# Optimization experiments

Measured on AMD Instinct MI355X. Metric: run time of the kernel, lower is better.

The kernel has to match this reference:

```python
import jax, jax.numpy as jnp
import numpy as np

N, E, C, A, F = 10000, 128000, 128, 10, 8
LDIMS = (1, 3, 5)  # 0e, 1o, 2e spherical-harmonic block sizes
NPATH = len(LDIMS)


def setup_inputs() -> dict:
    key = jax.random.key(0)
    ks = jax.random.split(key, 16)
    rn = lambda k, s, sc=1.0: jax.random.normal(k, s, dtype=jnp.float32) * sc
    inp = {
        "node_attrs": rn(ks[0], (N, A)),
        "node_feats": rn(ks[1], (N, C)),
        "edge_attrs_real": rn(ks[2], (E, 9)),
        "edge_attrs_imag": rn(ks[3], (E, 9)),
        "edge_feats": jax.random.uniform(ks[4], (E, F), dtype=jnp.float32),
        "edge_index": jax.random.randint(ks[5], (2, E), 0, N, dtype=jnp.int32),
        # learned parameters (e3nn 1/sqrt(fan_in) normalization folded into init)
        "W_up": rn(ks[6], (C, C), 1.0 / np.sqrt(C)),            # o3.Linear on 128x0e
        "W_skip": rn(ks[7], (C, A, C), 1.0 / np.sqrt(C * A)),    # FullyConnectedTensorProduct
        "W_mlp1": rn(ks[8], (F, 64), 1.0 / np.sqrt(F)),
        "W_mlp2": rn(ks[9], (64, 64), 1.0 / 8.0),
        "W_mlp3": rn(ks[10], (64, 64), 1.0 / 8.0),
        "W_mlp4": rn(ks[11], (64, NPATH * C), 1.0 / 8.0),        # -> conv_tp.weight_numel = 384
        "W_lin0": rn(ks[12], (C, C), 1.0 / np.sqrt(C)),          # o3.Linear per-l blocks
        "W_lin1": rn(ks[13], (C, C), 1.0 / np.sqrt(C)),
        "W_lin2": rn(ks[14], (C, C), 1.0 / np.sqrt(C)),
    }
    return inp


def _conv_tp(x, y, w):
    """scalar(128x0e) x sh(0e+1o+2e) uvu tensor product with per-edge weights.
    x: [E,C] sender scalars, y: [E,9] edge sh, w: [E,NPATH,C] -> [E, C*9] irreps_mid layout."""
    outs, off = [], 0
    for l, d in enumerate(LDIMS):
        yl = y[:, off:off + d]                      # [E,d]
        off += d
        xw = x * w[:, l]                            # [E,C]
        outs.append((xw[:, :, None] * yl[:, None, :]).reshape(-1, C * d))
    return jnp.concatenate(outs, axis=-1)           # [E, C*(1+3+5)]


def _linear_irreps(m, Ws):
    """o3.Linear mixing channels within each l block. m: [N, C*9] -> [N, C, 9]."""
    outs, off = [], 0
    for l, d in enumerate(LDIMS):
        blk = m[:, off:off + C * d].reshape(-1, C, d)  # [N,C,d]
        off += C * d
        outs.append(jnp.einsum('num,uk->nkm', blk, Ws[l]))
    return jnp.concatenate(outs, axis=-1)              # [N,C,9] (reshape_irreps layout)


def reference(node_attrs, node_feats, edge_attrs_real, edge_attrs_imag, edge_feats,
              edge_index, W_up, W_skip, W_mlp1, W_mlp2, W_mlp3, W_mlp4,
              W_lin0, W_lin1, W_lin2):
    sender, receiver = edge_index[0], edge_index[1]
    # skip connection: FullyConnectedTensorProduct(node_feats 128x0e, node_attrs 10x0e)
    sc = jnp.einsum('nu,nv,uvk->nk', node_feats, node_attrs, W_skip)
    # linear_up
    h = node_feats @ W_up
    # per-edge tensor-product weights from radial MLP (silu hidden layers, linear out)
    t = jax.nn.silu(edge_feats @ W_mlp1)
    t = jax.nn.silu(t @ W_mlp2)
    t = jax.nn.silu(t @ W_mlp3)
    tpw = (t @ W_mlp4).reshape(-1, NPATH, C)
    # gather senders, tensor product for real and imag edge attrs
    xs = h[sender]
    mji_r = _conv_tp(xs, edge_attrs_real, tpw)
    mji_i = _conv_tp(xs, edge_attrs_imag, tpw)
    # scatter-sum to receivers
    msg_r = jax.ops.segment_sum(mji_r, receiver, num_segments=N)
    msg_i = jax.ops.segment_sum(mji_i, receiver, num_segments=N)
    # output linear + reshape_irreps -> [N, C, 9]
    Ws = (W_lin0, W_lin1, W_lin2)
    out_r = _linear_irreps(msg_r, Ws)
    out_i = _linear_irreps(msg_i, Ws)
    return out_r, out_i, sc
```

## Files before the change

kernel.cpp:

```cpp
#include <hip/hip_runtime.h>
#include <hip/hip_bf16.h>

#define N_NODES 10000
#define N_EDGES 128000
#define C_DIM   128

typedef __attribute__((ext_vector_type(8))) short bf16x8;
typedef __attribute__((ext_vector_type(4))) float f32x4;


__device__ __forceinline__ float silu_f(float x) {
  return x / (1.f + __expf(-x));
}

__device__ __forceinline__ unsigned short f2bf(float x) {
  __hip_bfloat16 b = __float2bfloat16(x);
  return *(unsigned short*)&b;
}

__device__ __forceinline__ float bf2f(unsigned short u) {
  __hip_bfloat16 b = *(__hip_bfloat16*)&u;
  return __bfloat162float(b);
}

__device__ __forceinline__ bf16x8 pack8(float4 lo, float4 hi) {
  bf16x8 r;
  r[0] = (short)f2bf(lo.x); r[1] = (short)f2bf(lo.y);
  r[2] = (short)f2bf(lo.z); r[3] = (short)f2bf(lo.w);
  r[4] = (short)f2bf(hi.x); r[5] = (short)f2bf(hi.y);
  r[6] = (short)f2bf(hi.z); r[7] = (short)f2bf(hi.w);
  return r;
}

#define HB_NODES 40
__global__ __launch_bounds__(256) void k_h(const float* __restrict__ feats,
                                           const float* __restrict__ Wup,
                                           float* __restrict__ h) {
  int tid = threadIdx.x;
  int j = tid & 127;
  int par = tid >> 7;
  int n0 = blockIdx.x * HB_NODES;
  float wreg[128];
  #pragma unroll
  for (int k = 0; k < 128; k++) wreg[k] = Wup[k * 128 + j];
  #pragma unroll 2
  for (int i = par; i < HB_NODES; i += 2) {
    int n = __builtin_amdgcn_readfirstlane(n0 + i);
    const float* fr = &feats[n * 128];
    float acc = 0.f;
    #pragma unroll
    for (int k = 0; k < 128; k++) acc += fr[k] * wreg[k];
    h[n * 128 + j] = acc;
  }
}

__global__ void k_wcvt(const float* __restrict__ Wskip,
                       const float* __restrict__ Wl0,
                       const float* __restrict__ Wl1,
                       const float* __restrict__ Wl2,
                       const float* __restrict__ W1, const float* __restrict__ W2,
                       const float* __restrict__ W3, const float* __restrict__ W4,
                       unsigned short* __restrict__ wbT,
                       unsigned short* __restrict__ wlT,
                       unsigned short* __restrict__ w1f, unsigned short* __restrict__ w2f,
                       unsigned short* __restrict__ w3f, unsigned short* __restrict__ w4f) {
  int idx = blockIdx.x * 256 + threadIdx.x;
  if (idx < 163840) {
    int j = idx >> 7, k = idx & 127;
    int u = j / 10, v = j - u * 10;
    wbT[k * 1280 + v * 128 + u] = f2bf(Wskip[idx]);
  } else if (idx < 212992) {
    int t = idx - 163840;
    int l = t >> 14, r = t & 16383;
    int u = r >> 7, k = r & 127;
    const float* W = (l == 0) ? Wl0 : (l == 1) ? Wl1 : Wl2;
    wlT[(l * 128 + k) * 128 + u] = f2bf(W[r]);
  } else if (idx < 215040) {
    int j = idx - 212992;
    int ct = j >> 9, r = j & 511, n = r >> 5, t = r & 31;
    w1f[j] = (t < 8) ? f2bf(W1[t * 64 + ct * 16 + n]) : (unsigned short)0;
    (void)ct;
    if (t < 8) w1f[j] = f2bf(W1[t * 64 + ct * 16 + n]);
  } else if (idx < 219136) {
    int j = idx - 215040;
    int ctks = j >> 9, r = j & 511, n = r >> 5, t = r & 31;
    int ct = ctks >> 1, ks = ctks & 1;
    w2f[j] = f2bf(W2[(ks * 32 + t) * 64 + ct * 16 + n]);
  } else if (idx < 223232) {
    int j = idx - 219136;
    int ctks = j >> 9, r = j & 511, n = r >> 5, t = r & 31;
    int ct = ctks >> 1, ks = ctks & 1;
    w3f[j] = f2bf(W3[(ks * 32 + t) * 64 + ct * 16 + n]);
  } else if (idx < 247808) {
    int j = idx - 223232;
    int ctks = j >> 9, r = j & 511, n = r >> 5, t = r & 31;
    int ct = ctks >> 1, ks = ctks & 1;
    w4f[j] = f2bf(W4[(ks * 32 + t) * 384 + ct * 16 + n]);
  }
}

__global__ __launch_bounds__(256) void k_sc(const float* __restrict__ f,
                                            const float* __restrict__ at,
                                            const unsigned short* __restrict__ wbT,
                                            float* __restrict__ sc_out) {
  int tid = threadIdx.x;
  int w = tid >> 6, lane = tid & 63;
  int l15 = lane & 15, quad = lane >> 4;
  int n0 = blockIdx.x * 32;

  int nrow[2];
  #pragma unroll
  for (int t = 0; t < 2; t++) {
    int n = n0 + 16 * t + l15;
    nrow[t] = (n < N_NODES) ? n : (N_NODES - 1);
  }
  float4 fA[2][4][2];
  #pragma unroll
  for (int t = 0; t < 2; t++)
    #pragma unroll
    for (int ks = 0; ks < 4; ks++) {
      fA[t][ks][0] = *(const float4*)&f[nrow[t] * 128 + ks * 32 + quad * 8];
      fA[t][ks][1] = *(const float4*)&f[nrow[t] * 128 + ks * 32 + quad * 8 + 4];
    }

  f32x4 acc[2][2] = {};
  #pragma unroll 1
  for (int c = 0; c < 10; c++) {
    float av[2];
    #pragma unroll
    for (int t = 0; t < 2; t++) av[t] = at[nrow[t] * 10 + c];
    bf16x8 af[2][4];
    #pragma unroll
    for (int t = 0; t < 2; t++)
      #pragma unroll
      for (int ks = 0; ks < 4; ks++) {
        float4 lo = fA[t][ks][0], hi = fA[t][ks][1];
        lo.x *= av[t]; lo.y *= av[t]; lo.z *= av[t]; lo.w *= av[t];
        hi.x *= av[t]; hi.y *= av[t]; hi.z *= av[t]; hi.w *= av[t];
        af[t][ks] = pack8(lo, hi);
      }
    #pragma unroll
    for (int kt = 0; kt < 2; kt++) {
      int kcol = w * 32 + kt * 16 + l15;
      #pragma unroll
      for (int ks = 0; ks < 4; ks++) {
        bf16x8 bf = *(const bf16x8*)&wbT[kcol * 1280 + c * 128 + ks * 32 + quad * 8];
        #pragma unroll
        for (int t = 0; t < 2; t++)
          acc[t][kt] = __builtin_amdgcn_mfma_f32_16x16x32_bf16(af[t][ks], bf,
                                                               acc[t][kt], 0, 0, 0);
      }
    }
  }
  #pragma unroll
  for (int t = 0; t < 2; t++)
    #pragma unroll
    for (int kt = 0; kt < 2; kt++) {
      int kcol = w * 32 + kt * 16 + l15;
      #pragma unroll
      for (int reg = 0; reg < 4; reg++) {
        int n = n0 + 16 * t + quad * 4 + reg;
        if (n < N_NODES)
          __builtin_nontemporal_store(acc[t][kt][reg], &sc_out[n * 128 + kcol]);
      }
    }
}

__global__ __launch_bounds__(256) void k_mlp(const float* __restrict__ ef,
                                             const int* __restrict__ order,
                                             const unsigned short* __restrict__ w1f,
                                             const unsigned short* __restrict__ w2f,
                                             const unsigned short* __restrict__ w3f,
                                             const unsigned short* __restrict__ w4f,
                                             unsigned short* __restrict__ tpw) {
  __shared__ unsigned short sA[128][72];
  __shared__ unsigned short sB[128][72];
  int tid = threadIdx.x;
  int w = tid >> 6, lane = tid & 63;
  int l15 = lane & 15, quad = lane >> 4;
  int e0 = blockIdx.x * 128;
  int fragoff = l15 * 32 + quad * 8;
  int rb = w * 32;

  {
    bf16x8 af[2];
    #pragma unroll
    for (int rt = 0; rt < 2; rt++) {
      bf16x8 a = {};
      if (quad == 0) {
        int pos = e0 + rb + rt * 16 + l15;
        int e = order[pos];
        float4 lo = *(const float4*)&ef[e * 8];
        float4 hi = *(const float4*)&ef[e * 8 + 4];
        a = pack8(lo, hi);
      }
      af[rt] = a;
    }
    f32x4 ac[2][4] = {};
    #pragma unroll
    for (int ct = 0; ct < 4; ct++) {
      bf16x8 b = *(const bf16x8*)&w1f[ct * 512 + fragoff];
      ac[0][ct] = __builtin_amdgcn_mfma_f32_16x16x32_bf16(af[0], b, ac[0][ct], 0, 0, 0);
      ac[1][ct] = __builtin_amdgcn_mfma_f32_16x16x32_bf16(af[1], b, ac[1][ct], 0, 0, 0);
    }
    #pragma unroll
    for (int rt = 0; rt < 2; rt++)
      #pragma unroll
      for (int ct = 0; ct < 4; ct++)
        #pragma unroll
        for (int reg = 0; reg < 4; reg++)
          sA[rb + rt * 16 + quad * 4 + reg][ct * 16 + l15] =
              f2bf(silu_f(ac[rt][ct][reg]));
  }
  asm volatile("" ::: "memory");

  #pragma unroll 1
  for (int layer = 0; layer < 2; layer++) {
    unsigned short (*src)[72] = (layer == 0) ? sA : sB;
    unsigned short (*dst)[72] = (layer == 0) ? sB : sA;
    const unsigned short* wf = (layer == 0) ? w2f : w3f;
    bf16x8 a2[2][2];
    #pragma unroll
    for (int rt = 0; rt < 2; rt++)
      #pragma unroll
      for (int ks = 0; ks < 2; ks++)
        a2[rt][ks] = *(const bf16x8*)&src[rb + rt * 16 + l15][ks * 32 + quad * 8];
    f32x4 ac[2][4] = {};
    #pragma unroll
    for (int ct = 0; ct < 4; ct++)
      #pragma unroll
      for (int ks = 0; ks < 2; ks++) {
        bf16x8 b = *(const bf16x8*)&wf[(ct * 2 + ks) * 512 + fragoff];
        ac[0][ct] = __builtin_amdgcn_mfma_f32_16x16x32_bf16(a2[0][ks], b, ac[0][ct], 0, 0, 0);
        ac[1][ct] = __builtin_amdgcn_mfma_f32_16x16x32_bf16(a2[1][ks], b, ac[1][ct], 0, 0, 0);
      }
    #pragma unroll
    for (int rt = 0; rt < 2; rt++)
      #pragma unroll
      for (int ct = 0; ct < 4; ct++)
        #pragma unroll
        for (int reg = 0; reg < 4; reg++)
          dst[rb + rt * 16 + quad * 4 + reg][ct * 16 + l15] =
              f2bf(silu_f(ac[rt][ct][reg]));
    asm volatile("" ::: "memory");
  }

  bf16x8 a4[2][2];
  #pragma unroll
  for (int rt = 0; rt < 2; rt++)
    #pragma unroll
    for (int ks = 0; ks < 2; ks++)
      a4[rt][ks] = *(const bf16x8*)&sA[rb + rt * 16 + l15][ks * 32 + quad * 8];

  #pragma unroll 1
  for (int ch = 0; ch < 6; ch++) {
    f32x4 ac[2][4] = {};
    #pragma unroll
    for (int ct = 0; ct < 4; ct++)
      #pragma unroll
      for (int ks = 0; ks < 2; ks++) {
        bf16x8 b = *(const bf16x8*)&w4f[((ch * 4 + ct) * 2 + ks) * 512 + fragoff];
        ac[0][ct] = __builtin_amdgcn_mfma_f32_16x16x32_bf16(a4[0][ks], b, ac[0][ct], 0, 0, 0);
        ac[1][ct] = __builtin_amdgcn_mfma_f32_16x16x32_bf16(a4[1][ks], b, ac[1][ct], 0, 0, 0);
      }
    #pragma unroll
    for (int rt = 0; rt < 2; rt++)
      #pragma unroll
      for (int ct = 0; ct < 4; ct++)
        #pragma unroll
        for (int reg = 0; reg < 4; reg++)
          sB[rb + rt * 16 + quad * 4 + reg][ct * 16 + l15] = f2bf(ac[rt][ct][reg]);
    asm volatile("" ::: "memory");
    #pragma unroll
    for (int v = 0; v < 4; v++) {
      int idx = v * 64 + lane;
      int r = idx >> 3, cg = idx & 7;
      uint4 p = *(const uint4*)&sB[rb + r][cg * 8];
      *(uint4*)&tpw[(size_t)(e0 + rb + r) * 384 + ch * 64 + cg * 8] = p;
    }
    asm volatile("" ::: "memory");
  }
}

__global__ void k_hist(const int* __restrict__ recv, int* __restrict__ counts) {
  int e = blockIdx.x * 256 + threadIdx.x;
  if (e < N_EDGES) atomicAdd(&counts[recv[e]], 1);
}

__global__ __launch_bounds__(1024) void k_scan(const int* __restrict__ counts,
                                               int* __restrict__ offsets,
                                               int* __restrict__ cursor) {
  __shared__ int swave[16];
  int tid = threadIdx.x;
  int lane = tid & 63, w = tid >> 6;
  int base = tid * 10;
  int local[10]; int s = 0;
  #pragma unroll
  for (int i = 0; i < 10; i++) {
    int idx = base + i;
    int c = (idx < N_NODES) ? counts[idx] : 0;
    local[i] = s; s += c;
  }
  int inc = s;
  #pragma unroll
  for (int d = 1; d < 64; d <<= 1) {
    int v = __shfl_up(inc, d, 64);
    if (lane >= d) inc += v;
  }
  if (lane == 63) swave[w] = inc;
  __syncthreads();
  if (w == 0) {
    int t = (lane < 16) ? swave[lane] : 0;
    #pragma unroll
    for (int d = 1; d < 16; d <<= 1) {
      int v = __shfl_up(t, d, 64);
      if (lane >= d) t += v;
    }
    if (lane < 16) swave[lane] = t;
  }
  __syncthreads();
  int wpre = (w > 0) ? swave[w - 1] : 0;
  int pre = wpre + (inc - s);
  #pragma unroll
  for (int i = 0; i < 10; i++) {
    int idx = base + i;
    if (idx < N_NODES) { int o = pre + local[i]; offsets[idx] = o; cursor[idx] = o; }
  }
  if (tid == 1023) offsets[N_NODES] = wpre + inc;
}

__global__ void k_scatter(const int* __restrict__ recv, const int* __restrict__ send,
                          const float* __restrict__ yr, const float* __restrict__ yi,
                          int* __restrict__ cursor, int* __restrict__ order,
                          float* __restrict__ y2, int* __restrict__ ss) {
  int e = blockIdx.x * 256 + threadIdx.x;
  if (e < N_EDGES) {
    int idx = atomicAdd(&cursor[recv[e]], 1);
    order[idx] = e;
    ss[idx] = send[e];
    float* yy = &y2[(size_t)idx * 20];
    #pragma unroll
    for (int m = 0; m < 9; m++) {
      yy[m] = yr[e * 9 + m];
      yy[9 + m] = yi[e * 9 + m];
    }
    yy[18] = 0.f; yy[19] = 0.f;
  }
}

__device__ __forceinline__ void edge_fma(const float* __restrict__ y2, int pos,
                                         float xv, float t0, float t1, float t2,
                                         float* mr, float* mi) {
  const float* yy = &y2[(size_t)pos * 20];
  float4 v0 = *(const float4*)&yy[0];
  float4 v1 = *(const float4*)&yy[4];
  float4 v2 = *(const float4*)&yy[8];
  float4 v3 = *(const float4*)&yy[12];
  float2 v4 = *(const float2*)&yy[16];
  float xw0 = xv * t0, xw1 = xv * t1, xw2 = xv * t2;
  mr[0] += xw0 * v0.x;
  mr[1] += xw1 * v0.y; mr[2] += xw1 * v0.z; mr[3] += xw1 * v0.w;
  mr[4] += xw2 * v1.x; mr[5] += xw2 * v1.y; mr[6] += xw2 * v1.z;
  mr[7] += xw2 * v1.w; mr[8] += xw2 * v2.x;
  mi[0] += xw0 * v2.y;
  mi[1] += xw1 * v2.z; mi[2] += xw1 * v2.w; mi[3] += xw1 * v3.x;
  mi[4] += xw2 * v3.y; mi[5] += xw2 * v3.z; mi[6] += xw2 * v3.w;
  mi[7] += xw2 * v4.x; mi[8] += xw2 * v4.y;
}

__global__ __launch_bounds__(128, 6) void k_gather(
    const float* __restrict__ h, const unsigned short* __restrict__ tpw,
    const float* __restrict__ y2, const int* __restrict__ ss,
    const int* __restrict__ offsets,
    unsigned short* __restrict__ msg) {
  int u = threadIdx.x;
  int n = blockIdx.x;
  float mr[9] = {}, mi[9] = {};
  int e0 = __builtin_amdgcn_readfirstlane(offsets[n]);
  int e1 = __builtin_amdgcn_readfirstlane(offsets[n + 1]);
  int jj = e0;
  for (; jj + 3 < e1; jj += 4) {
    float xv[4], t0[4], t1[4], t2[4];
    #pragma unroll
    for (int q = 0; q < 4; q++) {
      int pos = jj + q;
      int s = ss[pos];
      const unsigned short* tp = &tpw[(size_t)pos * 384 + u];
      t0[q] = bf2f(__builtin_nontemporal_load(tp));
      t1[q] = bf2f(__builtin_nontemporal_load(tp + 128));
      t2[q] = bf2f(__builtin_nontemporal_load(tp + 256));
      xv[q] = h[s * 128 + u];
    }
    #pragma unroll
    for (int q = 0; q < 4; q++)
      edge_fma(y2, jj + q, xv[q], t0[q], t1[q], t2[q], mr, mi);
  }
  for (; jj < e1; jj++) {
    int s = ss[jj];
    const unsigned short* tp = &tpw[(size_t)jj * 384 + u];
    float t0 = bf2f(__builtin_nontemporal_load(tp));
    float t1 = bf2f(__builtin_nontemporal_load(tp + 128));
    float t2 = bf2f(__builtin_nontemporal_load(tp + 256));
    float xv = h[s * 128 + u];
    edge_fma(y2, jj, xv, t0, t1, t2, mr, mi);
  }
  int g = n >> 3, i = n & 7;
  unsigned short* mg = msg + (size_t)g * 144 * 128;
  mg[(i * 2 + 0) * 128 + u] = f2bf(mr[0]);
  mg[(i * 2 + 1) * 128 + u] = f2bf(mi[0]);
  #pragma unroll
  for (int m = 1; m < 4; m++) {
    mg[(16 + i * 6 + (m - 1)) * 128 + u] = f2bf(mr[m]);
    mg[(16 + i * 6 + 3 + (m - 1)) * 128 + u] = f2bf(mi[m]);
  }
  #pragma unroll
  for (int m = 4; m < 9; m++) {
    mg[(64 + i * 10 + (m - 4)) * 128 + u] = f2bf(mr[m]);
    mg[(64 + i * 10 + 5 + (m - 4)) * 128 + u] = f2bf(mi[m]);
  }
}

#define LIN_ROWPAD 1156
__global__ __launch_bounds__(256) void k_lin(const unsigned short* __restrict__ msg,
                                             const unsigned short* __restrict__ wlT,
                                             float* __restrict__ out) {
  __shared__ float so[2 * 8 * LIN_ROWPAD];
  int tid = threadIdx.x;
  int w = tid >> 6, lane = tid & 63;
  int l15 = lane & 15, quad = lane >> 4;
  int g = blockIdx.x;

  bf16x8 bfr[3][2][4];
  #pragma unroll
  for (int l = 0; l < 3; l++)
    #pragma unroll
    for (int kt = 0; kt < 2; kt++)
      #pragma unroll
      for (int ks = 0; ks < 4; ks++) {
        int ncol = w * 32 + kt * 16 + l15;
        bfr[l][kt][ks] = *(const bf16x8*)&wlT[(l * 128 + ncol) * 128 + ks * 32 + quad * 8];
      }

  const unsigned short* mg = msg + (size_t)g * 144 * 128;

  #pragma unroll
  for (int tile = 0; tile < 9; tile++) {
    const int l = (tile == 0) ? 0 : (tile < 4) ? 1 : 2;
    const int rbase = tile * 16;
    bf16x8 af[4];
    #pragma unroll
    for (int ks = 0; ks < 4; ks++)
      af[ks] = *(const bf16x8*)&mg[(rbase + l15) * 128 + ks * 32 + quad * 8];
    f32x4 acc0 = {}, acc1 = {};
    #pragma unroll
    for (int ks = 0; ks < 4; ks++) {
      acc0 = __builtin_amdgcn_mfma_f32_16x16x32_bf16(af[ks], bfr[l][0][ks], acc0, 0, 0, 0);
      acc1 = __builtin_amdgcn_mfma_f32_16x16x32_bf16(af[ks], bfr[l][1][ks], acc1, 0, 0, 0);
    }
    #pragma unroll
    for (int reg = 0; reg < 4; reg++) {
      int r = rbase + quad * 4 + reg;
      int c, ni, m;
      if (tile == 0) { ni = (r & 15) >> 1; c = r & 1; m = 0; }
      else if (tile < 4) {
        int q = r - 16; ni = q / 6; int rem = q - ni * 6;
        c = rem >= 3; m = 1 + rem - (c ? 3 : 0);
      } else {
        int q = r - 64; ni = q / 10; int rem = q - ni * 10;
        c = rem >= 5; m = 4 + rem - (c ? 5 : 0);
      }
      int k0 = w * 32 + l15;
      float* ob = &so[(c * 8 + ni) * LIN_ROWPAD + m];
      ob[(k0)      * 9] = acc0[reg];
      ob[(k0 + 16) * 9] = acc1[reg];
    }
  }
  __syncthreads();
  #pragma unroll
  for (int v = 0; v < 18; v++) {
    int idx = v * 256 + tid;
    int c = idx / 2304;
    int rem = idx - c * 2304;
    int ni = rem / 288;
    int off4 = rem - ni * 288;
    f32x4 p = *(const f32x4*)&so[(c * 8 + ni) * LIN_ROWPAD + off4 * 4];
    f32x4* dst = (f32x4*)&out[(size_t)c * 11520000 + ((size_t)g * 8 + ni) * 1152 +
                              (size_t)off4 * 4];
    __builtin_nontemporal_store(p, dst);
  }
}

extern "C" void kernel_launch(void* const* d_in, const int* in_sizes, int n_in,
                              void* d_out, int out_size, void* d_ws, size_t ws_size,
                              hipStream_t stream) {
  const float* node_attrs = (const float*)d_in[0];
  const float* node_feats = (const float*)d_in[1];
  const float* ear   = (const float*)d_in[2];
  const float* eai   = (const float*)d_in[3];
  const float* ef    = (const float*)d_in[4];
  const int*   eidx  = (const int*)d_in[5];
  const float* Wup   = (const float*)d_in[6];
  const float* Wskip = (const float*)d_in[7];
  const float* W1    = (const float*)d_in[8];
  const float* W2    = (const float*)d_in[9];
  const float* W3    = (const float*)d_in[10];
  const float* W4    = (const float*)d_in[11];
  const float* Wl0   = (const float*)d_in[12];
  const float* Wl1   = (const float*)d_in[13];
  const float* Wl2   = (const float*)d_in[14];
  float* out = (float*)d_out;

  char* ws = (char*)d_ws;
  float*          h       = (float*)ws;
  unsigned short* tpw     = (unsigned short*)(ws + 5120000);
  unsigned short* msg     = (unsigned short*)(ws + 103424000);
  unsigned short* wlT     = (unsigned short*)(ws + 149504000);
  unsigned short* wbT     = (unsigned short*)(ws + 149602304);
  int*            counts  = (int*)(ws + 149929984);
  int*            offsets = (int*)(ws + 149969984);
  int*            cursor  = (int*)(ws + 150010112);
  int*            order   = (int*)(ws + 150050112);
  unsigned short* w1f     = (unsigned short*)(ws + 150562816);
  unsigned short* w2f     = (unsigned short*)(ws + 150566912);
  unsigned short* w3f     = (unsigned short*)(ws + 150575104);
  unsigned short* w4f     = (unsigned short*)(ws + 150583296);

  float* y2 = (float*)d_out;
  int*   ss = (int*)((char*)d_out + 10240000);

  const int* send = eidx;
  const int* recv = eidx + N_EDGES;

  hipMemsetAsync(counts, 0, N_NODES * sizeof(int), stream);
  k_hist<<<dim3(500), dim3(256), 0, stream>>>(recv, counts);
  k_scan<<<dim3(1), dim3(1024), 0, stream>>>(counts, offsets, cursor);
  k_scatter<<<dim3(500), dim3(256), 0, stream>>>(recv, send, ear, eai, cursor,
                                                 order, y2, ss);
  k_wcvt<<<dim3(968), dim3(256), 0, stream>>>(Wskip, Wl0, Wl1, Wl2,
                                              W1, W2, W3, W4,
                                              wbT, wlT, w1f, w2f, w3f, w4f);
  k_h<<<dim3(250), dim3(256), 0, stream>>>(node_feats, Wup, h);
  k_sc<<<dim3(313), dim3(256), 0, stream>>>(node_feats, node_attrs, wbT,
                                            out + 2 * 11520000);
  k_mlp<<<dim3(1000), dim3(256), 0, stream>>>(ef, order, w1f, w2f, w3f, w4f, tpw);
  k_gather<<<dim3(10000), dim3(128), 0, stream>>>(h, tpw, y2, ss, offsets, msg);
  k_lin<<<dim3(1250), dim3(256), 0, stream>>>(msg, wlT, out);
  (void)in_sizes; (void)n_in; (void)out_size; (void)ws_size;
}
```

Before: 335.0 us.

## Fuse gather-scatter aggregation with output linear via shared-memory message tile

Merges k_gather and k_lin into one kernel. Each 256-thread block aggregates messages for 8 nodes, with two 128-thread teams taking 4 nodes each, writes them as bf16 into shared memory, then runs the MFMA output linear directly from LDS. This removes the global msg round trip and one launch. Because y2/ss can no longer alias the output buffer, they move into the workspace. The trade-off is far fewer, larger blocks (1250 instead of 10000) with heavy LDS use and launch_bounds(256,1), so the memory-bound gather phase has less parallelism to hide latency.

```diff
diff --git a/kernel.cpp b/kernel.cpp
--- a/kernel.cpp
+++ b/kernel.cpp
@@ -79,8 +79,6 @@
     int j = idx - 212992;
     int ct = j >> 9, r = j & 511, n = r >> 5, t = r & 31;
     w1f[j] = (t < 8) ? f2bf(W1[t * 64 + ct * 16 + n]) : (unsigned short)0;
-    (void)ct;
-    if (t < 8) w1f[j] = f2bf(W1[t * 64 + ct * 16 + n]);
   } else if (idx < 219136) {
     int j = idx - 215040;
     int ctks = j >> 9, r = j & 511, n = r >> 5, t = r & 31;
@@ -347,6 +345,9 @@
     yy[18] = 0.f; yy[19] = 0.f;
   }
 }
+
+#define SMSG_PAD 136
+#define LIN_ROWPAD 1156
 
 __device__ __forceinline__ void edge_fma(const float* __restrict__ y2, int pos,
                                          float xv, float t0, float t1, float t2,
@@ -368,125 +369,130 @@
   mi[7] += xw2 * v4.x; mi[8] += xw2 * v4.y;
 }
 
-__global__ __launch_bounds__(128, 6) void k_gather(
+__global__ __launch_bounds__(256, 1) void k_gl(
     const float* __restrict__ h, const unsigned short* __restrict__ tpw,
     const float* __restrict__ y2, const int* __restrict__ ss,
     const int* __restrict__ offsets,
-    unsigned short* __restrict__ msg) {
-  int u = threadIdx.x;
-  int n = blockIdx.x;
-  float mr[9] = {}, mi[9] = {};
-  int e0 = __builtin_amdgcn_readfirstlane(offsets[n]);
-  int e1 = __builtin_amdgcn_readfirstlane(offsets[n + 1]);
-  int jj = e0;
-  for (; jj + 3 < e1; jj += 4) {
-    float xv[4], t0[4], t1[4], t2[4];
-    #pragma unroll
-    for (int q = 0; q < 4; q++) {
-      int pos = jj + q;
-      int s = ss[pos];
-      const unsigned short* tp = &tpw[(size_t)pos * 384 + u];
-      t0[q] = bf2f(__builtin_nontemporal_load(tp));
-      t1[q] = bf2f(__builtin_nontemporal_load(tp + 128));
-      t2[q] = bf2f(__builtin_nontemporal_load(tp + 256));
-      xv[q] = h[s * 128 + u];
-    }
-    #pragma unroll
-    for (int q = 0; q < 4; q++)
-      edge_fma(y2, jj + q, xv[q], t0[q], t1[q], t2[q], mr, mi);
-  }
-  for (; jj < e1; jj++) {
-    int s = ss[jj];
-    const unsigned short* tp = &tpw[(size_t)jj * 384 + u];
-    float t0 = bf2f(__builtin_nontemporal_load(tp));
-    float t1 = bf2f(__builtin_nontemporal_load(tp + 128));
-    float t2 = bf2f(__builtin_nontemporal_load(tp + 256));
-    float xv = h[s * 128 + u];
-    edge_fma(y2, jj, xv, t0, t1, t2, mr, mi);
-  }
-  int g = n >> 3, i = n & 7;
-  unsigned short* mg = msg + (size_t)g * 144 * 128;
-  mg[(i * 2 + 0) * 128 + u] = f2bf(mr[0]);
-  mg[(i * 2 + 1) * 128 + u] = f2bf(mi[0]);
-  #pragma unroll
-  for (int m = 1; m < 4; m++) {
-    mg[(16 + i * 6 + (m - 1)) * 128 + u] = f2bf(mr[m]);
-    mg[(16 + i * 6 + 3 + (m - 1)) * 128 + u] = f2bf(mi[m]);
-  }
-  #pragma unroll
-  for (int m = 4; m < 9; m++) {
-    mg[(64 + i * 10 + (m - 4)) * 128 + u] = f2bf(mr[m]);
-    mg[(64 + i * 10 + 5 + (m - 4)) * 128 + u] = f2bf(mi[m]);
-  }
-}
-
-#define LIN_ROWPAD 1156
-__global__ __launch_bounds__(256) void k_lin(const unsigned short* __restrict__ msg,
-                                             const unsigned short* __restrict__ wlT,
-                                             float* __restrict__ out) {
+    const unsigned short* __restrict__ wlT,
+    float* __restrict__ out) {
+  __shared__ unsigned short smsg[144 * SMSG_PAD];
   __shared__ float so[2 * 8 * LIN_ROWPAD];
   int tid = threadIdx.x;
-  int w = tid >> 6, lane = tid & 63;
-  int l15 = lane & 15, quad = lane >> 4;
   int g = blockIdx.x;
 
-  bf16x8 bfr[3][2][4];
-  #pragma unroll
-  for (int l = 0; l < 3; l++)
-    #pragma unroll
-    for (int kt = 0; kt < 2; kt++)
+  {
+    int u = tid & 127;
+    int team = tid >> 7;
+    #pragma unroll 1
+    for (int t = 0; t < 4; t++) {
+      int i = team * 4 + t;
+      int n = g * 8 + i;
+      float mr[9] = {}, mi[9] = {};
+      int e0 = __builtin_amdgcn_readfirstlane(offsets[n]);
+      int e1 = __builtin_amdgcn_readfirstlane(offsets[n + 1]);
+      int jj = e0;
+      for (; jj + 3 < e1; jj += 4) {
+        float xv[4], t0[4], t1[4], t2[4];
+        #pragma unroll
+        for (int q = 0; q < 4; q++) {
+          int pos = jj + q;
+          int s = ss[pos];
+          const unsigned short* tp = &tpw[(size_t)pos * 384 + u];
+          t0[q] = bf2f(__builtin_nontemporal_load(tp));
+          t1[q] = bf2f(__builtin_nontemporal_load(tp + 128));
+          t2[q] = bf2f(__builtin_nontemporal_load(tp + 256));
+          xv[q] = h[s * 128 + u];
+        }
+        #pragma unroll
+        for (int q = 0; q < 4; q++)
+          edge_fma(y2, jj + q, xv[q], t0[q], t1[q], t2[q], mr, mi);
+      }
+      for (; jj < e1; jj++) {
+        int s = ss[jj];
+        const unsigned short* tp = &tpw[(size_t)jj * 384 + u];
+        float t0 = bf2f(__builtin_nontemporal_load(tp));
+        float t1 = bf2f(__builtin_nontemporal_load(tp + 128));
+        float t2 = bf2f(__builtin_nontemporal_load(tp + 256));
+        float xv = h[s * 128 + u];
+        edge_fma(y2, jj, xv, t0, t1, t2, mr, mi);
+      }
+      smsg[(i * 2 + 0) * SMSG_PAD + u] = f2bf(mr[0]);
+      smsg[(i * 2 + 1) * SMSG_PAD + u] = f2bf(mi[0]);
+      #pragma unroll
+      for (int m = 1; m < 4; m++) {
+        smsg[(16 + i * 6 + (m - 1)) * SMSG_PAD + u] = f2bf(mr[m]);
+        smsg[(16 + i * 6 + 3 + (m - 1)) * SMSG_PAD + u] = f2bf(mi[m]);
+      }
+      #pragma unroll
+      for (int m = 4; m < 9; m++) {
+        smsg[(64 + i * 10 + (m - 4)) * SMSG_PAD + u] = f2bf(mr[m]);
+        smsg[(64 + i * 10 + 5 + (m - 4)) * SMSG_PAD + u] = f2bf(mi[m]);
+      }
+    }
+  }
+  __syncthreads();
+
+  {
+    int w = tid >> 6, lane = tid & 63;
+    int l15 = lane & 15, quad = lane >> 4;
+
+    bf16x8 bfr[3][2][4];
+    #pragma unroll
+    for (int l = 0; l < 3; l++)
+      #pragma unroll
+      for (int kt = 0; kt < 2; kt++)
+        #pragma unroll
+        for (int ks = 0; ks < 4; ks++) {
+          int ncol = w * 32 + kt * 16 + l15;
+          bfr[l][kt][ks] =
+              *(const bf16x8*)&wlT[(l * 128 + ncol) * 128 + ks * 32 + quad * 8];
+        }
+
+    #pragma unroll
+    for (int tile = 0; tile < 9; tile++) {
+      const int l = (tile == 0) ? 0 : (tile < 4) ? 1 : 2;
+      const int rbase = tile * 16;
+      bf16x8 af[4];
+      #pragma unroll
+      for (int ks = 0; ks < 4; ks++)
+        af[ks] = *(const bf16x8*)&smsg[(rbase + l15) * SMSG_PAD + ks * 32 + quad * 8];
+      f32x4 acc0 = {}, acc1 = {};
       #pragma unroll
       for (int ks = 0; ks < 4; ks++) {
-        int ncol = w * 32 + kt * 16 + l15;
-        bfr[l][kt][ks] = *(const bf16x8*)&wlT[(l * 128 + ncol) * 128 + ks * 32 + quad * 8];
-      }
-
-  const unsigned short* mg = msg + (size_t)g * 144 * 128;
-
-  #pragma unroll
-  for (int tile = 0; tile < 9; tile++) {
-    const int l = (tile == 0) ? 0 : (tile < 4) ? 1 : 2;
-    const int rbase = tile * 16;
-    bf16x8 af[4];
-    #pragma unroll
-    for (int ks = 0; ks < 4; ks++)
-      af[ks] = *(const bf16x8*)&mg[(rbase + l15) * 128 + ks * 32 + quad * 8];
-    f32x4 acc0 = {}, acc1 = {};
-    #pragma unroll
-    for (int ks = 0; ks < 4; ks++) {
-      acc0 = __builtin_amdgcn_mfma_f32_16x16x32_bf16(af[ks], bfr[l][0][ks], acc0, 0, 0, 0);
-      acc1 = __builtin_amdgcn_mfma_f32_16x16x32_bf16(af[ks], bfr[l][1][ks], acc1, 0, 0, 0);
-    }
-    #pragma unroll
-    for (int reg = 0; reg < 4; reg++) {
-      int r = rbase + quad * 4 + reg;
-      int c, ni, m;
-      if (tile == 0) { ni = (r & 15) >> 1; c = r & 1; m = 0; }
-      else if (tile < 4) {
-        int q = r - 16; ni = q / 6; int rem = q - ni * 6;
-        c = rem >= 3; m = 1 + rem - (c ? 3 : 0);
-      } else {
-        int q = r - 64; ni = q / 10; int rem = q - ni * 10;
-        c = rem >= 5; m = 4 + rem - (c ? 5 : 0);
-      }
-      int k0 = w * 32 + l15;
-      float* ob = &so[(c * 8 + ni) * LIN_ROWPAD + m];
-      ob[(k0)      * 9] = acc0[reg];
-      ob[(k0 + 16) * 9] = acc1[reg];
-    }
-  }
-  __syncthreads();
-  #pragma unroll
-  for (int v = 0; v < 18; v++) {
-    int idx = v * 256 + tid;
-    int c = idx / 2304;
-    int rem = idx - c * 2304;
-    int ni = rem / 288;
-    int off4 = rem - ni * 288;
-    f32x4 p = *(const f32x4*)&so[(c * 8 + ni) * LIN_ROWPAD + off4 * 4];
-    f32x4* dst = (f32x4*)&out[(size_t)c * 11520000 + ((size_t)g * 8 + ni) * 1152 +
-                              (size_t)off4 * 4];
-    __builtin_nontemporal_store(p, dst);
+        acc0 = __builtin_amdgcn_mfma_f32_16x16x32_bf16(af[ks], bfr[l][0][ks], acc0, 0, 0, 0);
+        acc1 = __builtin_amdgcn_mfma_f32_16x16x32_bf16(af[ks], bfr[l][1][ks], acc1, 0, 0, 0);
+      }
+      #pragma unroll
+      for (int reg = 0; reg < 4; reg++) {
+        int r = rbase + quad * 4 + reg;
+        int c, ni, m;
+        if (tile == 0) { ni = (r & 15) >> 1; c = r & 1; m = 0; }
+        else if (tile < 4) {
+          int q = r - 16; ni = q / 6; int rem = q - ni * 6;
+          c = rem >= 3; m = 1 + rem - (c ? 3 : 0);
+        } else {
+          int q = r - 64; ni = q / 10; int rem = q - ni * 10;
+          c = rem >= 5; m = 4 + rem - (c ? 5 : 0);
+        }
+        int k0 = w * 32 + l15;
+        float* ob = &so[(c * 8 + ni) * LIN_ROWPAD + m];
+        ob[(k0)      * 9] = acc0[reg];
+        ob[(k0 + 16) * 9] = acc1[reg];
+      }
+    }
+    __syncthreads();
+    #pragma unroll
+    for (int v = 0; v < 18; v++) {
+      int idx = v * 256 + tid;
+      int c = idx / 2304;
+      int rem = idx - c * 2304;
+      int ni = rem / 288;
+      int off4 = rem - ni * 288;
+      f32x4 p = *(const f32x4*)&so[(c * 8 + ni) * LIN_ROWPAD + off4 * 4];
+      f32x4* dst = (f32x4*)&out[(size_t)c * 11520000 + ((size_t)g * 8 + ni) * 1152 +
+                                (size_t)off4 * 4];
+      __builtin_nontemporal_store(p, dst);
+    }
   }
 }
 
@@ -513,7 +519,8 @@
   char* ws = (char*)d_ws;
   float*          h       = (float*)ws;
   unsigned short* tpw     = (unsigned short*)(ws + 5120000);
-  unsigned short* msg     = (unsigned short*)(ws + 103424000);
+  float*          y2      = (float*)(ws + 103424000);
+  int*            ss      = (int*)(ws + 113664000);
   unsigned short* wlT     = (unsigned short*)(ws + 149504000);
   unsigned short* wbT     = (unsigned short*)(ws + 149602304);
   int*            counts  = (int*)(ws + 149929984);
@@ -524,9 +531,6 @@
   unsigned short* w2f     = (unsigned short*)(ws + 150566912);
   unsigned short* w3f     = (unsigned short*)(ws + 150575104);
   unsigned short* w4f     = (unsigned short*)(ws + 150583296);
-
-  float* y2 = (float*)d_out;
-  int*   ss = (int*)((char*)d_out + 10240000);
 
   const int* send = eidx;
   const int* recv = eidx + N_EDGES;
@@ -543,7 +547,6 @@
   k_sc<<<dim3(313), dim3(256), 0, stream>>>(node_feats, node_attrs, wbT,
                                             out + 2 * 11520000);
   k_mlp<<<dim3(1000), dim3(256), 0, stream>>>(ef, order, w1f, w2f, w3f, w4f, tpw);
-  k_gather<<<dim3(10000), dim3(128), 0, stream>>>(h, tpw, y2, ss, offsets, msg);
-  k_lin<<<dim3(1250), dim3(256), 0, stream>>>(msg, wlT, out);
+  k_gl<<<dim3(1250), dim3(256), 0, stream>>>(h, tpw, y2, ss, offsets, wlT, out);
   (void)in_sizes; (void)n_in; (void)out_size; (void)ws_size;
 }
```

After: 516.3 us. 1.54x slower.
